# Kernel optimization log

Measured on AMD Instinct MI355X. Metric: run time of the kernel, lower is better.

The kernel has to match this reference:

```python
import jax, jax.numpy as jnp
import numpy as np

UNITS = 256

def setup_inputs() -> dict:
    key = jax.random.key(0)
    k1, k2, k3, k4 = jax.random.split(key, 4)
    B, T, F = 131072, 7, 60
    x = jax.random.normal(k1, (B, T, F), dtype=jnp.float32)
    W = jax.random.normal(k2, (F, 4 * UNITS), dtype=jnp.float32) * 0.05
    U = jax.random.normal(k3, (UNITS, 4 * UNITS), dtype=jnp.float32) * 0.05
    b = jax.random.normal(k4, (4 * UNITS,), dtype=jnp.float32) * 0.05
    return {"x": x, "W": W, "U": U, "b": b}

def reference(x, W, U, b):
    # Keras LSTM, return_sequences=False, return_state=True -> (last_h, h, c).
    # Gate order in the fused kernel: i, f, c(g), o. Inference path (no dropout).
    B = x.shape[0]
    h0 = jnp.zeros((B, UNITS), dtype=x.dtype)
    c0 = jnp.zeros((B, UNITS), dtype=x.dtype)

    def step(carry, xt):
        h, c = carry
        z = xt @ W + h @ U + b  # [B, 4*UNITS]
        zi, zf, zg, zo = jnp.split(z, 4, axis=-1)
        i = jax.nn.sigmoid(zi)
        f = jax.nn.sigmoid(zf)
        g = jnp.tanh(zg)
        o = jax.nn.sigmoid(zo)
        c_new = f * c + i * g
        h_new = o * jnp.tanh(c_new)
        return (h_new, c_new), None

    xs = jnp.transpose(x, (1, 0, 2))  # [T, B, F]
    (h, c), _ = jax.lax.scan(step, (h0, c0), xs)
    return h, h, c
```

## Files before the change

### kernel.cpp

```cpp
#include <hip/hip_runtime.h>

typedef __bf16 bf16x8 __attribute__((ext_vector_type(8)));
typedef float f32x4 __attribute__((ext_vector_type(4)));

#define TSTEPS 7
#define FEAT 60
#define MTILE 64
#define THREADS 256

__global__ void prep_U_kernel(const float* __restrict__ U, __bf16* __restrict__ Ut) {
    int idx = blockIdx.x * blockDim.x + threadIdx.x;
    int n = idx >> 8;
    int k = idx & 255;
    Ut[idx] = (__bf16)U[k * 1024 + n];
}

__global__ void prep_W_kernel(const float* __restrict__ W, __bf16* __restrict__ Wt) {
    int idx = blockIdx.x * blockDim.x + threadIdx.x;
    int n = idx >> 6;
    int k = idx & 63;
    float v = (k < FEAT) ? W[k * 1024 + n] : 0.0f;
    Wt[idx] = (__bf16)v;
}

__device__ __forceinline__ float sigm(float z) {
    return __builtin_amdgcn_rcpf(1.0f + __expf(-z));
}
__device__ __forceinline__ float tanh_(float z) {
    return 1.0f - 2.0f * __builtin_amdgcn_rcpf(__expf(2.0f * z) + 1.0f);
}

__global__ __launch_bounds__(THREADS, 1)
void lstm_kernel(const float* __restrict__ x, const __bf16* __restrict__ Ut,
                 const __bf16* __restrict__ Wt, const float* __restrict__ bias,
                 float* __restrict__ out, int B) {
    __shared__ __align__(16) __bf16 x_lds[TSTEPS][MTILE][72];
    __shared__ __align__(16) __bf16 h_lds[MTILE][264];

    const int tid = threadIdx.x;
    const int wave = tid >> 6;
    const int lane = tid & 63;
    const int quad = lane >> 4;
    const int l16 = lane & 15;
    const int r0 = blockIdx.x * MTILE;

    for (int i = tid; i < MTILE * TSTEPS * FEAT; i += THREADS) {
        int m = i / (TSTEPS * FEAT);
        int rem = i - m * (TSTEPS * FEAT);
        int t = rem / FEAT;
        int f = rem - t * FEAT;
        x_lds[t][m][f] = (__bf16)x[(size_t)(r0 + m) * (TSTEPS * FEAT) + rem];
    }
    for (int i = tid; i < MTILE * TSTEPS * 4; i += THREADS) {
        int m = i / (TSTEPS * 4);
        int rem = i - m * (TSTEPS * 4);
        int t = rem >> 2;
        int f = FEAT + (rem & 3);
        x_lds[t][m][f] = (__bf16)0.0f;
    }

    float c_reg[4][4][4];
#pragma unroll
    for (int uc = 0; uc < 4; ++uc)
#pragma unroll
        for (int mt = 0; mt < 4; ++mt)
#pragma unroll
            for (int r = 0; r < 4; ++r) c_reg[uc][mt][r] = 0.0f;

    float bvals[4][4];
#pragma unroll
    for (int uc = 0; uc < 4; ++uc)
#pragma unroll
        for (int g = 0; g < 4; ++g)
            bvals[uc][g] = bias[g * 256 + wave * 64 + uc * 16 + l16];

    __syncthreads();

    const size_t HN = (size_t)B * 256;

    for (int t = 0; t < TSTEPS; ++t) {
        bf16x8 a[4][10];
        if (t > 0) {
#pragma unroll
            for (int mt = 0; mt < 4; ++mt)
#pragma unroll
                for (int kf = 0; kf < 8; ++kf)
                    a[mt][kf] = *(const bf16x8*)&h_lds[mt * 16 + l16][kf * 32 + quad * 8];
        }
#pragma unroll
        for (int mt = 0; mt < 4; ++mt) {
            a[mt][8] = *(const bf16x8*)&x_lds[t][mt * 16 + l16][quad * 8];
            a[mt][9] = *(const bf16x8*)&x_lds[t][mt * 16 + l16][32 + quad * 8];
        }
        __syncthreads();

#pragma unroll
        for (int uc = 0; uc < 4; ++uc) {
            const int ncol = wave * 64 + uc * 16 + l16;
            f32x4 acc[4];

            auto gate_gemm = [&](int g) {
                const __bf16* uRow = Ut + (size_t)(g * 256 + ncol) * 256;
                const __bf16* wRow = Wt + (size_t)(g * 256 + ncol) * 64;
                bf16x8 bfr[10];
                if (t > 0) {
#pragma unroll
                    for (int kf = 0; kf < 8; ++kf)
                        bfr[kf] = *(const bf16x8*)(uRow + kf * 32 + quad * 8);
                }
#pragma unroll
                for (int kf = 0; kf < 2; ++kf)
                    bfr[8 + kf] = *(const bf16x8*)(wRow + kf * 32 + quad * 8);
#pragma unroll
                for (int mt = 0; mt < 4; ++mt) acc[mt] = (f32x4){0.f, 0.f, 0.f, 0.f};
                if (t > 0) {
#pragma unroll
                    for (int kf = 0; kf < 8; ++kf)
#pragma unroll
                        for (int mt = 0; mt < 4; ++mt)
                            acc[mt] = __builtin_amdgcn_mfma_f32_16x16x32_bf16(
                                a[mt][kf], bfr[kf], acc[mt], 0, 0, 0);
                }
#pragma unroll
                for (int kf = 0; kf < 2; ++kf)
#pragma unroll
                    for (int mt = 0; mt < 4; ++mt)
                        acc[mt] = __builtin_amdgcn_mfma_f32_16x16x32_bf16(
                            a[mt][8 + kf], bfr[8 + kf], acc[mt], 0, 0, 0);
            };

            float iv[4][4], pg[4][4];
            gate_gemm(0);
#pragma unroll
            for (int mt = 0; mt < 4; ++mt)
#pragma unroll
                for (int r = 0; r < 4; ++r)
                    iv[mt][r] = sigm(acc[mt][r] + bvals[uc][0]);
            gate_gemm(2);
#pragma unroll
            for (int mt = 0; mt < 4; ++mt)
#pragma unroll
                for (int r = 0; r < 4; ++r)
                    pg[mt][r] = iv[mt][r] * tanh_(acc[mt][r] + bvals[uc][2]);
            gate_gemm(1);
#pragma unroll
            for (int mt = 0; mt < 4; ++mt)
#pragma unroll
                for (int r = 0; r < 4; ++r)
                    c_reg[uc][mt][r] =
                        sigm(acc[mt][r] + bvals[uc][1]) * c_reg[uc][mt][r] + pg[mt][r];
            gate_gemm(3);
#pragma unroll
            for (int mt = 0; mt < 4; ++mt)
#pragma unroll
                for (int r = 0; r < 4; ++r) {
                    float cc = c_reg[uc][mt][r];
                    float hv = sigm(acc[mt][r] + bvals[uc][3]) * tanh_(cc);
                    h_lds[mt * 16 + quad * 4 + r][ncol] = (__bf16)hv;
                    if (t == TSTEPS - 1) {
                        size_t mg = (size_t)(r0 + mt * 16 + quad * 4 + r);
                        out[mg * 256 + ncol] = hv;
                        out[HN + mg * 256 + ncol] = hv;
                        out[2 * HN + mg * 256 + ncol] = cc;
                    }
                }
        }
        __syncthreads();
    }
}

extern "C" void kernel_launch(void* const* d_in, const int* in_sizes, int n_in,
                              void* d_out, int out_size, void* d_ws, size_t ws_size,
                              hipStream_t stream) {
    const float* x = (const float*)d_in[0];
    const float* W = (const float*)d_in[1];
    const float* U = (const float*)d_in[2];
    const float* b = (const float*)d_in[3];
    float* out = (float*)d_out;

    const int B = in_sizes[0] / (TSTEPS * FEAT);

    __bf16* Ut = (__bf16*)d_ws;
    __bf16* Wt = (__bf16*)((char*)d_ws + 1024 * 256 * 2);

    prep_U_kernel<<<1024, 256, 0, stream>>>(U, Ut);
    prep_W_kernel<<<256, 256, 0, stream>>>(W, Wt);
    lstm_kernel<<<B / MTILE, THREADS, 0, stream>>>(x, Ut, Wt, b, out, B);
}
```

Baseline: 2.292 ms.

## Double-buffer per-timestep x staging and allow two blocks per CU

```diff
diff --git a/kernel.cpp b/kernel.cpp
--- a/kernel.cpp
+++ b/kernel.cpp
@@ -30,11 +30,11 @@
     return 1.0f - 2.0f * __builtin_amdgcn_rcpf(__expf(2.0f * z) + 1.0f);
 }
 
-__global__ __launch_bounds__(THREADS, 1)
+__global__ __launch_bounds__(THREADS, 2)
 void lstm_kernel(const float* __restrict__ x, const __bf16* __restrict__ Ut,
                  const __bf16* __restrict__ Wt, const float* __restrict__ bias,
                  float* __restrict__ out, int B) {
-    __shared__ __align__(16) __bf16 x_lds[TSTEPS][MTILE][72];
+    __shared__ __align__(16) __bf16 x_lds[2][MTILE][72];
     __shared__ __align__(16) __bf16 h_lds[MTILE][264];
 
     const int tid = threadIdx.x;
@@ -44,20 +44,27 @@
     const int l16 = lane & 15;
     const int r0 = blockIdx.x * MTILE;
 
-    for (int i = tid; i < MTILE * TSTEPS * FEAT; i += THREADS) {
-        int m = i / (TSTEPS * FEAT);
-        int rem = i - m * (TSTEPS * FEAT);
-        int t = rem / FEAT;
-        int f = rem - t * FEAT;
-        x_lds[t][m][f] = (__bf16)x[(size_t)(r0 + m) * (TSTEPS * FEAT) + rem];
+    for (int i = tid; i < 2 * MTILE * 4; i += THREADS) {
+        int bb = i >> 8;
+        int rem = i & 255;
+        x_lds[bb][rem >> 2][FEAT + (rem & 3)] = (__bf16)0.0f;
     }
-    for (int i = tid; i < MTILE * TSTEPS * 4; i += THREADS) {
-        int m = i / (TSTEPS * 4);
-        int rem = i - m * (TSTEPS * 4);
-        int t = rem >> 2;
-        int f = FEAT + (rem & 3);
-        x_lds[t][m][f] = (__bf16)0.0f;
-    }
+
+    auto stage_x = [&](int t, int b) {
+        for (int i = tid; i < MTILE * 15; i += THREADS) {
+            int m = i / 15;
+            int q = i - m * 15;
+            const float4 v =
+                *(const float4*)&x[((size_t)(r0 + m) * TSTEPS + t) * FEAT + q * 4];
+            __bf16* dst = &x_lds[b][m][q * 4];
+            dst[0] = (__bf16)v.x;
+            dst[1] = (__bf16)v.y;
+            dst[2] = (__bf16)v.z;
+            dst[3] = (__bf16)v.w;
+        }
+    };
+
+    stage_x(0, 0);
 
     float c_reg[4][4][4];
 #pragma unroll
@@ -79,6 +86,7 @@
     const size_t HN = (size_t)B * 256;
 
     for (int t = 0; t < TSTEPS; ++t) {
+        const int xb = t & 1;
         bf16x8 a[4][10];
         if (t > 0) {
 #pragma unroll
@@ -89,10 +97,12 @@
         }
 #pragma unroll
         for (int mt = 0; mt < 4; ++mt) {
-            a[mt][8] = *(const bf16x8*)&x_lds[t][mt * 16 + l16][quad * 8];
-            a[mt][9] = *(const bf16x8*)&x_lds[t][mt * 16 + l16][32 + quad * 8];
+            a[mt][8] = *(const bf16x8*)&x_lds[xb][mt * 16 + l16][quad * 8];
+            a[mt][9] = *(const bf16x8*)&x_lds[xb][mt * 16 + l16][32 + quad * 8];
         }
         __syncthreads();
+
+        if (t + 1 < TSTEPS) stage_x(t + 1, xb ^ 1);
 
 #pragma unroll
         for (int uc = 0; uc < 4; ++uc) {
```

Result: slower. 2.849 ms (+24.3%).
